# Performance work log

Measured on AMD Instinct MI355X. Metric: run time of the kernel, lower is better.

## Reference

```python
import jax, jax.numpy as jnp
import numpy as np

B, S, D = 2, 2048, 1024
H, DA, DL = 8, 64, 64   # heads, attention_dim, linear_dim
L = 2                    # num_blocks


def _layernorm(x, w, b, eps):
    mu = jnp.mean(x, axis=-1, keepdims=True)
    var = jnp.mean(jnp.square(x - mu), axis=-1, keepdims=True)
    return (x - mu) * jax.lax.rsqrt(var + eps) * w + b


def _norm_no_affine(x, eps):
    mu = jnp.mean(x, axis=-1, keepdims=True)
    var = jnp.mean(jnp.square(x - mu), axis=-1, keepdims=True)
    return (x - mu) * jax.lax.rsqrt(var + eps)


def setup_inputs() -> dict:
    key = jax.random.key(0)
    ks = jax.random.split(key, 8)
    x = jax.random.normal(ks[0], (B, S, D), dtype=jnp.float32)
    # causal visibility mask: True = visible
    attn_mask = jnp.tril(jnp.ones((S, S), dtype=bool))[None].repeat(B, axis=0)
    proj_dim = DL * 2 * H + DA * 2 * H  # 2048
    uvqk = jax.random.normal(ks[1], (L, D, proj_dim), dtype=jnp.float32) * 0.02
    o_w = jax.random.normal(ks[2], (L, D, DL * H), dtype=jnp.float32) * 0.02  # torch [out,in]
    o_b = jnp.zeros((L, D), dtype=jnp.float32)
    ln_w = jnp.ones((L, D), dtype=jnp.float32)
    ln_b = jnp.zeros((L, D), dtype=jnp.float32)
    last_ln_w = jnp.ones((D,), dtype=jnp.float32)
    last_ln_b = jnp.zeros((D,), dtype=jnp.float32)
    return {"x": x, "attn_mask": attn_mask, "uvqk": uvqk, "o_w": o_w,
            "o_b": o_b, "ln_w": ln_w, "ln_b": ln_b,
            "last_ln_w": last_ln_w, "last_ln_b": last_ln_b}


def reference(x, attn_mask, uvqk, o_w, o_b, ln_w, ln_b, last_ln_w, last_ln_b):
    seq_len = x.shape[1]
    m = attn_mask[:, None, :, :]  # [B,1,S,S]
    for i in range(L):
        h = _layernorm(x, ln_w[i], ln_b[i], 1e-6)                 # [B,S,D]
        proj = jax.nn.silu(jnp.einsum('bsd,de->bse', h, uvqk[i]))  # [B,S,2*(DL+DA)*H]
        u, v, q, k = jnp.split(proj, [DL * H, 2 * DL * H, 2 * DL * H + DA * H], axis=-1)
        q = q.reshape(B, seq_len, H, DA).transpose(0, 2, 1, 3)   # [B,H,S,DA]
        kk = k.reshape(B, seq_len, H, DA).transpose(0, 2, 1, 3)
        vv = v.reshape(B, seq_len, H, DL).transpose(0, 2, 1, 3)  # [B,H,S,DL]
        uu = u.reshape(B, seq_len, H, DL).transpose(0, 2, 1, 3)
        scores = jnp.einsum('bhsd,bhtd->bhst', q, kk)            # [B,H,S,S]
        scores = jnp.where(m, jax.nn.silu(scores) / seq_len, 0.0)
        out = jnp.einsum('bhst,bhtd->bhsd', scores, vv)          # [B,H,S,DL]
        out = _norm_no_affine(out, 1e-6)
        u_dot = (uu * out).transpose(0, 2, 1, 3).reshape(B, seq_len, DL * H)
        x = x + jnp.einsum('bsf,df->bsd', u_dot, o_w[i]) + o_b[i]
    return _layernorm(x, last_ln_w, last_ln_b, 1e-8)
```

## Files before the change

### kernel.cpp

```cpp
#include <hip/hip_runtime.h>

#define B_ 2
#define S_ 2048
#define D_ 1024
#define H_ 8
#define L_ 2
#define P_ 2048
#define F_ 512
#define R_ (B_*S_)

typedef unsigned short u16;
typedef unsigned int u32;
typedef __bf16 bf16;
typedef bf16 bf16x8 __attribute__((ext_vector_type(8)));
typedef short short8 __attribute__((ext_vector_type(8)));
typedef float v4f __attribute__((ext_vector_type(4)));

__device__ __forceinline__ float silu_fast(float x){
  float e = __expf(-x);
  return x * __builtin_amdgcn_rcpf(1.0f + e);
}
__device__ __forceinline__ float bf2f(u16 u){
  union { u32 i; float f; } x; x.i = ((u32)u) << 16; return x.f;
}
__device__ __forceinline__ u16 f2bfu(float f){
  union { float f; u32 i; } x; x.f = f;
  u32 r = x.i + 0x7fff + ((x.i >> 16) & 1);
  return (u16)(r >> 16);
}
__device__ __forceinline__ void gload16(const u16* g, u16* l){
  __builtin_amdgcn_global_load_lds(
      (const __attribute__((address_space(1))) void*)g,
      (__attribute__((address_space(3))) void*)l, 16, 0, 0);
}

__global__ __launch_bounds__(256) void cvt_bf16_kernel(const float* __restrict__ src, u16* __restrict__ dst){
  int i = (blockIdx.x * 256 + threadIdx.x) * 4;
  float4 v = *(const float4*)(src + i);
  ushort4 o; o.x = f2bfu(v.x); o.y = f2bfu(v.y); o.z = f2bfu(v.z); o.w = f2bfu(v.w);
  *(ushort4*)(dst + i) = o;
}

__global__ __launch_bounds__(256) void cvt_uvqkT_kernel(const float* __restrict__ uvqk, u16* __restrict__ ot){
  __shared__ float t[32][33];
  int l = blockIdx.z;
  int p0 = blockIdx.x * 32, d0 = blockIdx.y * 32;
  int tx = threadIdx.x & 31, ty = threadIdx.x >> 5;
  const float* src = uvqk + ((size_t)l * D_ + d0) * P_ + p0;
  #pragma unroll
  for (int s = 0; s < 4; s++)
    t[ty + s*8][tx] = src[(size_t)(ty + s*8) * P_ + tx];
  __syncthreads();
  u16* dst = ot + ((size_t)l * P_ + p0) * D_ + d0;
  #pragma unroll
  for (int s = 0; s < 4; s++)
    dst[(size_t)(ty + s*8) * D_ + tx] = f2bfu(t[tx][ty + s*8]);
}

__global__ __launch_bounds__(256) void kvpack_kernel(const u16* __restrict__ projh,
    u16* __restrict__ kpack, u16* __restrict__ vpack){
  __shared__ u16 tls[64*72];
  int t = blockIdx.x, t0 = t * 64;
  int bh = blockIdx.y;
  int b = bh >> 3, hh = bh & 7;
  int tid = threadIdx.x;
  const size_t bS = (size_t)b * S_;
  const int voff = F_ + hh*64, koff = 3*F_ + hh*64;
  {
    int row = tid >> 2, c16 = (tid & 3) * 16;
    const u16* sp = projh + (bS + t0 + row) * P_ + voff + c16;
    short8 a = *(const short8*)sp;
    short8 bq = *(const short8*)(sp + 8);
    *(short8*)&tls[row*72 + c16] = a;
    *(short8*)&tls[row*72 + c16 + 8] = bq;
  }
  __syncthreads();
  size_t obase = ((size_t)(bh*32 + t) * 8) * 512;
  #pragma unroll
  for (int pass = 0; pass < 2; pass++){
    int id = tid + pass * 256;
    int c = id >> 6, lane = id & 63;
    int quad = lane >> 4, l15 = lane & 15;
    int cns = c >> 1, ckst = c & 1;
    const u16* kp = projh + (bS + t0 + cns*16 + l15) * P_ + koff + ckst*32 + quad*8;
    *(short8*)(kpack + obase + (size_t)c*512 + lane*8) = *(const short8*)kp;
    short8 vv;
    #pragma unroll
    for (int j = 0; j < 8; j++)
      vv[j] = (short)tls[(ckst*32 + quad*8 + j)*72 + cns*16 + l15];
    *(short8*)(vpack + obase + (size_t)c*512 + lane*8) = vv;
  }
}

__global__ __launch_bounds__(256) void ln_kernel(const float* __restrict__ src,
    const float* __restrict__ w, const float* __restrict__ b,
    void* __restrict__ outp, float eps, int out_bf16){
  int row = blockIdx.x, tid = threadIdx.x;
  const float* xr = src + (size_t)row * D_;
  float4 v = *(const float4*)(xr + tid * 4);
  float s  = v.x + v.y + v.z + v.w;
  float sq = v.x*v.x + v.y*v.y + v.z*v.z + v.w*v.w;
  #pragma unroll
  for (int off = 32; off; off >>= 1){ s += __shfl_down(s, off); sq += __shfl_down(sq, off); }
  __shared__ float red[8];
  __shared__ float stats[2];
  int wid = tid >> 6;
  if ((tid & 63) == 0){ red[wid] = s; red[4 + wid] = sq; }
  __syncthreads();
  if (tid == 0){
    float S1 = red[0] + red[1] + red[2] + red[3];
    float S2 = red[4] + red[5] + red[6] + red[7];
    float mu = S1 * (1.0f / D_);
    float var = S2 * (1.0f / D_) - mu * mu;
    stats[0] = mu; stats[1] = rsqrtf(var + eps);
  }
  __syncthreads();
  float mu = stats[0], rs = stats[1];
  int i = tid * 4;
  float4 wv = *(const float4*)(w + i);
  float4 bv = *(const float4*)(b + i);
  float o0 = (v.x - mu) * rs * wv.x + bv.x;
  float o1 = (v.y - mu) * rs * wv.y + bv.y;
  float o2 = (v.z - mu) * rs * wv.z + bv.z;
  float o3 = (v.w - mu) * rs * wv.w + bv.w;
  if (out_bf16){
    ushort4 o; o.x = f2bfu(o0); o.y = f2bfu(o1); o.z = f2bfu(o2); o.w = f2bfu(o3);
    *(ushort4*)((u16*)outp + (size_t)row * D_ + i) = o;
  } else {
    *(float4*)((float*)outp + (size_t)row * D_ + i) = make_float4(o0, o1, o2, o3);
  }
}

template<int KDIM>
__device__ __forceinline__ void gemm_mfma_core(const u16* __restrict__ A,
    const u16* __restrict__ Bt, u16* As, u16* Bs, int m0, int n0, v4f acc[4][4]){
  int tid = threadIdx.x;
  int w = tid >> 6, lane = tid & 63;
  int wm = w >> 1, wn = w & 1, quad = lane >> 4, l15 = lane & 15;
  int srow = lane >> 2, skoct = (lane & 3) * 8;
  for (int kt = 0; kt < KDIM; kt += 32){
    __syncthreads();
    #pragma unroll
    for (int s = 0; s < 2; s++){
      int g = w * 2 + s;
      gload16(A  + (size_t)(m0 + g*16 + srow) * KDIM + kt + skoct, As + g*512);
      gload16(Bt + (size_t)(n0 + g*16 + srow) * KDIM + kt + skoct, Bs + g*512);
    }
    __syncthreads();
    short8 af[4], bfr[4];
    #pragma unroll
    for (int i = 0; i < 4; i++)
      af[i] = *(const short8*)&As[(wm*64 + i*16 + l15)*32 + quad*8];
    #pragma unroll
    for (int j = 0; j < 4; j++)
      bfr[j] = *(const short8*)&Bs[(wn*64 + j*16 + l15)*32 + quad*8];
    #pragma unroll
    for (int i = 0; i < 4; i++)
      #pragma unroll
      for (int j = 0; j < 4; j++)
        acc[i][j] = __builtin_amdgcn_mfma_f32_16x16x32_bf16(
            __builtin_bit_cast(bf16x8, af[i]), __builtin_bit_cast(bf16x8, bfr[j]),
            acc[i][j], 0, 0, 0);
  }
}

__global__ __launch_bounds__(256) void gemm_silu_mfma(const u16* __restrict__ A,
    const u16* __restrict__ Bt, u16* __restrict__ C){
  __shared__ u16 As[128*32], Bs[128*32];
  v4f acc[4][4];
  #pragma unroll
  for (int i = 0; i < 4; i++)
    #pragma unroll
    for (int j = 0; j < 4; j++) acc[i][j] = (v4f){0.f,0.f,0.f,0.f};
  int f = blockIdx.x;
  int wg = (f & 7) * 64 + (f >> 3);
  int bx = wg & 15, by = wg >> 4;
  int m0 = by * 128, n0 = bx * 128;
  gemm_mfma_core<D_>(A, Bt, As, Bs, m0, n0, acc);
  int tid = threadIdx.x, w = tid >> 6, lane = tid & 63;
  int wm = w >> 1, wn = w & 1, quad = lane >> 4, l15 = lane & 15;
  #pragma unroll
  for (int i = 0; i < 4; i++)
    #pragma unroll
    for (int r = 0; r < 4; r++){
      int m = m0 + wm*64 + i*16 + quad*4 + r;
      u16* cp = C + (size_t)m * P_ + n0 + wn*64 + l15;
      #pragma unroll
      for (int j = 0; j < 4; j++)
        cp[j*16] = f2bfu(silu_fast(acc[i][j][r]));
    }
}

__global__ __launch_bounds__(256) void gemm_add_mfma(const u16* __restrict__ A,
    const u16* __restrict__ Bt, const float* __restrict__ bias,
    const float* __restrict__ Xin, float* __restrict__ Xout){
  __shared__ u16 As[128*32], Bs[128*32];
  v4f acc[4][4];
  #pragma unroll
  for (int i = 0; i < 4; i++)
    #pragma unroll
    for (int j = 0; j < 4; j++) acc[i][j] = (v4f){0.f,0.f,0.f,0.f};
  int f = blockIdx.x;
  int wg = (f & 7) * 32 + (f >> 3);
  int bx = wg & 7, by = wg >> 3;
  int m0 = by * 128, n0 = bx * 128;
  gemm_mfma_core<F_>(A, Bt, As, Bs, m0, n0, acc);
  int tid = threadIdx.x, w = tid >> 6, lane = tid & 63;
  int wm = w >> 1, wn = w & 1, quad = lane >> 4, l15 = lane & 15;
  float bj[4];
  #pragma unroll
  for (int j = 0; j < 4; j++) bj[j] = bias[n0 + wn*64 + j*16 + l15];
  #pragma unroll
  for (int i = 0; i < 4; i++)
    #pragma unroll
    for (int r = 0; r < 4; r++){
      int m = m0 + wm*64 + i*16 + quad*4 + r;
      size_t off = (size_t)m * D_ + n0 + wn*64 + l15;
      const float* xi = Xin + off;
      float* xo = Xout + off;
      #pragma unroll
      for (int j = 0; j < 4; j++)
        xo[j*16] = xi[j*16] + acc[i][j][r] + bj[j];
    }
}

__global__ __launch_bounds__(256) void attn_kernel(const u16* __restrict__ projh,
                                                   const u16* __restrict__ kpack,
                                                   const u16* __restrict__ vpack,
                                                   u16* __restrict__ opart){
  __shared__ u16 Ps[64*72];
  int f = (int)blockIdx.x;
  int g = f & 7;
  int s = f >> 3;
  int c = s & 31;
  int slot = s >> 5;
  int z = c >> 4;
  int x = c & 15;
  int qt = slot ? x : (15 - x);
  int bh = g + (slot << 3);
  int ttop = 2*qt + 1;
  int b = bh >> 3, hh = bh & 7;
  int tid = threadIdx.x;
  int w = tid >> 6, lane = tid & 63, quad = lane >> 4, l15 = lane & 15;
  int s0 = qt * 128;
  const size_t bS = (size_t)b * S_;
  const int qoff = 2*F_ + hh*64;

  bf16x8 aq[2][2];
  #pragma unroll
  for (int qh = 0; qh < 2; qh++){
    const u16* qp = projh + (bS + s0 + qh*64 + w*16 + l15) * P_ + qoff + quad*8;
    aq[qh][0] = __builtin_bit_cast(bf16x8, *(const short8*)qp);
    aq[qh][1] = __builtin_bit_cast(bf16x8, *(const short8*)(qp + 32));
  }

  v4f oacc[2][4];
  #pragma unroll
  for (int qh = 0; qh < 2; qh++)
    #pragma unroll
    for (int i = 0; i < 4; i++) oacc[qh][i] = (v4f){0.f, 0.f, 0.f, 0.f};

  auto LOADT = [&](short8 (&BK)[4][2], short8 (&VF)[4][2], int tt){
    size_t pb = ((size_t)(bh*32 + tt) * 8) * 512;
    #pragma unroll
    for (int cc = 0; cc < 8; cc++){
      BK[cc>>1][cc&1] = *(const short8*)(kpack + pb + (size_t)cc*512 + lane*8);
      VF[cc>>1][cc&1] = *(const short8*)(vpack + pb + (size_t)cc*512 + lane*8);
    }
  };

  auto COMPUTE = [&](const short8 (&BK)[4][2], const short8 (&VF)[4][2], int t){
    #pragma unroll
    for (int qh = 0; qh < 2; qh++){
      int dtile = 2*qt + qh;
      if (t > dtile) continue;
      v4f sacc[4];
      #pragma unroll
      for (int i = 0; i < 4; i++) sacc[i] = (v4f){0.f, 0.f, 0.f, 0.f};
      #pragma unroll
      for (int ns = 0; ns < 4; ns++){
        sacc[ns] = __builtin_amdgcn_mfma_f32_16x16x32_bf16(aq[qh][0],
            __builtin_bit_cast(bf16x8, BK[ns][0]), sacc[ns], 0, 0, 0);
        sacc[ns] = __builtin_amdgcn_mfma_f32_16x16x32_bf16(aq[qh][1],
            __builtin_bit_cast(bf16x8, BK[ns][1]), sacc[ns], 0, 0, 0);
      }
      bool diag = (t == dtile);
      #pragma unroll
      for (int ns = 0; ns < 4; ns++){
        #pragma unroll
        for (int r = 0; r < 4; r++){
          int rl = w*16 + quad*4 + r;
          int cl = ns*16 + l15;
          float p = silu_fast(sacc[ns][r]) * (1.0f / S_);
          if (diag && cl > rl) p = 0.0f;
          Ps[rl*72 + cl] = f2bfu(p);
        }
      }
      #pragma unroll
      for (int kst = 0; kst < 2; kst++){
        short8 aps = *(const short8*)&Ps[(w*16 + l15)*72 + kst*32 + quad*8];
        bf16x8 ap = __builtin_bit_cast(bf16x8, aps);
        #pragma unroll
        for (int ds = 0; ds < 4; ds++)
          oacc[qh][ds] = __builtin_amdgcn_mfma_f32_16x16x32_bf16(
              ap, __builtin_bit_cast(bf16x8, VF[ds][kst]), oacc[qh][ds], 0, 0, 0);
      }
    }
  };

  short8 kA[4][2], vA[4][2], kB[4][2], vB[4][2];
  int t = z;
  LOADT(kA, vA, t);
  for (;;){
    if (t + 2 <= ttop){
      LOADT(kB, vB, t + 2);
      COMPUTE(kA, vA, t);
      t += 2;
    } else {
      COMPUTE(kA, vA, t);
      break;
    }
    if (t + 2 <= ttop){
      LOADT(kA, vA, t + 2);
      COMPUTE(kB, vB, t);
      t += 2;
    } else {
      COMPUTE(kB, vB, t);
      break;
    }
  }

  u16* ob = opart + (size_t)z * ((size_t)R_ * F_);
  #pragma unroll
  for (int qh = 0; qh < 2; qh++){
    #pragma unroll
    for (int r = 0; r < 4; r++){
      int sg = s0 + qh*64 + w*16 + quad*4 + r;
      u16* op = ob + (bS + sg) * (size_t)F_ + hh*64 + l15;
      #pragma unroll
      for (int ds = 0; ds < 4; ds++)
        op[ds*16] = f2bfu(oacc[qh][ds][r]);
    }
  }
}

__global__ __launch_bounds__(256) void norm_gate_kernel(const u16* __restrict__ opart,
    const u16* __restrict__ projh, u16* __restrict__ udot){
  int w = threadIdx.x >> 6, lane = threadIdx.x & 63;
  int sg = blockIdx.x * 4 + w;
  int hh = lane >> 3, seg = lane & 7;
  size_t off = (size_t)sg * F_ + hh*64 + seg*8;
  short8 a0 = *(const short8*)(opart + off);
  short8 a1 = *(const short8*)(opart + (size_t)R_ * F_ + off);
  float e[8];
  float s = 0.f, sq = 0.f;
  #pragma unroll
  for (int i = 0; i < 8; i++){
    e[i] = bf2f((u16)a0[i]) + bf2f((u16)a1[i]);
    s += e[i]; sq += e[i]*e[i];
  }
  #pragma unroll
  for (int m = 1; m < 8; m <<= 1){
    s  += __shfl_xor(s, m, 64);
    sq += __shfl_xor(sq, m, 64);
  }
  float mu = s * (1.0f/64.0f);
  float var = sq * (1.0f/64.0f) - mu*mu;
  float rs = rsqrtf(var + 1e-6f);
  const u16* up = projh + (size_t)sg * P_ + hh*64 + seg*8;
  short8 uv = *(const short8*)up;
  short8 ov;
  #pragma unroll
  for (int i = 0; i < 8; i++)
    ov[i] = (short)f2bfu((e[i] - mu) * rs * bf2f((u16)uv[i]));
  *(short8*)(udot + off) = ov;
}

extern "C" void kernel_launch(void* const* d_in, const int* in_sizes, int n_in,
                              void* d_out, int out_size, void* d_ws, size_t ws_size,
                              hipStream_t stream){
  (void)in_sizes; (void)n_in; (void)out_size; (void)ws_size;
  const float* x     = (const float*)d_in[0];
  const float* uvqk  = (const float*)d_in[2];
  const float* o_w   = (const float*)d_in[3];
  const float* o_b   = (const float*)d_in[4];
  const float* ln_w  = (const float*)d_in[5];
  const float* ln_b  = (const float*)d_in[6];
  const float* lln_w = (const float*)d_in[7];
  const float* lln_b = (const float*)d_in[8];
  float* out = (float*)d_out;

  char* ws = (char*)d_ws;
  float* xf    = (float*)ws;
  u16*   h     = (u16*)(ws + (16u<<20));
  u16*   kpack = h;
  u16*   vpack = (u16*)(ws + (20u<<20));
  u16*   udot  = (u16*)(ws + (24u<<20));
  u16*   projh = (u16*)(ws + (28u<<20));
  u16*   uvqkT = (u16*)(ws + (44u<<20));
  u16*   owh   = (u16*)(ws + (52u<<20));
  u16*   opart = (u16*)(ws + (54u<<20));

  cvt_uvqkT_kernel<<<dim3(P_/32, D_/32, L_), 256, 0, stream>>>(uvqk, uvqkT);
  cvt_bf16_kernel<<<L_ * D_ * F_ / 1024, 256, 0, stream>>>(o_w, owh);
  for (int l = 0; l < L_; l++){
    const float* xsrc = (l == 0) ? x : xf;
    ln_kernel<<<R_, 256, 0, stream>>>(xsrc, ln_w + l * D_, ln_b + l * D_, h, 1e-6f, 1);
    gemm_silu_mfma<<<512, 256, 0, stream>>>(
        h, uvqkT + (size_t)l * P_ * D_, projh);
    kvpack_kernel<<<dim3(S_/64, B_*H_), 256, 0, stream>>>(projh, kpack, vpack);
    attn_kernel<<<512, 256, 0, stream>>>(projh, kpack, vpack, opart);
    norm_gate_kernel<<<R_/4, 256, 0, stream>>>(opart, projh, udot);
    gemm_add_mfma<<<256, 256, 0, stream>>>(
        udot, owh + (size_t)l * D_ * F_, o_b + l * D_, xsrc, xf);
  }
  ln_kernel<<<R_, 256, 0, stream>>>(xf, lln_w, lln_b, out, 1e-8f, 0);
}
```

Baseline: 280.1 us.

## Load GEMM operands directly into registers with double buffering, remap blocks per XCD

Replaces the LDS-staged GEMM core (global_load_lds plus two barriers per k-step) with per-wave direct global-to-register loads of MFMA fragments, double-buffered across k-steps so loads overlap compute. It also changes the block-to-tile mapping so each of the 8 XCDs gets a contiguous 2D patch of output tiles, aiming for better L2 reuse. This removes LDS traffic and barriers, but each wave now fetches its own A/B fragments, so there is no intra-block sharing and global/L2 traffic goes up, with strided 16-byte loads per lane.

```diff
diff --git a/kernel.cpp b/kernel.cpp
--- a/kernel.cpp
+++ b/kernel.cpp
@@ -27,11 +27,6 @@
   union { float f; u32 i; } x; x.f = f;
   u32 r = x.i + 0x7fff + ((x.i >> 16) & 1);
   return (u16)(r >> 16);
-}
-__device__ __forceinline__ void gload16(const u16* g, u16* l){
-  __builtin_amdgcn_global_load_lds(
-      (const __attribute__((address_space(1))) void*)g,
-      (__attribute__((address_space(3))) void*)l, 16, 0, 0);
 }
 
 __global__ __launch_bounds__(256) void cvt_bf16_kernel(const float* __restrict__ src, u16* __restrict__ dst){
@@ -132,53 +127,52 @@
 }
 
 template<int KDIM>
-__device__ __forceinline__ void gemm_mfma_core(const u16* __restrict__ A,
-    const u16* __restrict__ Bt, u16* As, u16* Bs, int m0, int n0, v4f acc[4][4]){
-  int tid = threadIdx.x;
-  int w = tid >> 6, lane = tid & 63;
-  int wm = w >> 1, wn = w & 1, quad = lane >> 4, l15 = lane & 15;
-  int srow = lane >> 2, skoct = (lane & 3) * 8;
-  for (int kt = 0; kt < KDIM; kt += 32){
-    __syncthreads();
-    #pragma unroll
-    for (int s = 0; s < 2; s++){
-      int g = w * 2 + s;
-      gload16(A  + (size_t)(m0 + g*16 + srow) * KDIM + kt + skoct, As + g*512);
-      gload16(Bt + (size_t)(n0 + g*16 + srow) * KDIM + kt + skoct, Bs + g*512);
-    }
-    __syncthreads();
-    short8 af[4], bfr[4];
-    #pragma unroll
-    for (int i = 0; i < 4; i++)
-      af[i] = *(const short8*)&As[(wm*64 + i*16 + l15)*32 + quad*8];
-    #pragma unroll
-    for (int j = 0; j < 4; j++)
-      bfr[j] = *(const short8*)&Bs[(wn*64 + j*16 + l15)*32 + quad*8];
+__device__ __forceinline__ void gemm_reg_core(const u16* __restrict__ A,
+    const u16* __restrict__ Bt, int m0w, int n0w, v4f acc[4][4]){
+  int lane = threadIdx.x & 63, quad = lane >> 4, l15 = lane & 15;
+  const u16* ap = A  + (size_t)(m0w + l15) * KDIM + quad*8;
+  const u16* bp = Bt + (size_t)(n0w + l15) * KDIM + quad*8;
+  short8 aA[4], bA[4], aB[4], bB[4];
+  auto LOADK = [&](short8 (&af)[4], short8 (&bf)[4], int kt){
+    #pragma unroll
+    for (int i = 0; i < 4; i++){
+      af[i] = *(const short8*)(ap + (size_t)i*16*KDIM + kt);
+      bf[i] = *(const short8*)(bp + (size_t)i*16*KDIM + kt);
+    }
+  };
+  auto COMP = [&](const short8 (&af)[4], const short8 (&bf)[4]){
     #pragma unroll
     for (int i = 0; i < 4; i++)
       #pragma unroll
       for (int j = 0; j < 4; j++)
         acc[i][j] = __builtin_amdgcn_mfma_f32_16x16x32_bf16(
-            __builtin_bit_cast(bf16x8, af[i]), __builtin_bit_cast(bf16x8, bfr[j]),
+            __builtin_bit_cast(bf16x8, af[i]), __builtin_bit_cast(bf16x8, bf[j]),
             acc[i][j], 0, 0, 0);
+  };
+  LOADK(aA, bA, 0);
+  for (int kt = 0; kt < KDIM; kt += 64){
+    if (kt + 32 < KDIM) LOADK(aB, bB, kt + 32);
+    COMP(aA, bA);
+    if (kt + 64 < KDIM) LOADK(aA, bA, kt + 64);
+    COMP(aB, bB);
   }
 }
 
 __global__ __launch_bounds__(256) void gemm_silu_mfma(const u16* __restrict__ A,
     const u16* __restrict__ Bt, u16* __restrict__ C){
-  __shared__ u16 As[128*32], Bs[128*32];
   v4f acc[4][4];
   #pragma unroll
   for (int i = 0; i < 4; i++)
     #pragma unroll
     for (int j = 0; j < 4; j++) acc[i][j] = (v4f){0.f,0.f,0.f,0.f};
   int f = blockIdx.x;
-  int wg = (f & 7) * 64 + (f >> 3);
-  int bx = wg & 15, by = wg >> 4;
+  int k = f & 7, local = f >> 3;
+  int by = (k & 3) * 8 + (local >> 3);
+  int bx = (k >> 2) * 8 + (local & 7);
   int m0 = by * 128, n0 = bx * 128;
-  gemm_mfma_core<D_>(A, Bt, As, Bs, m0, n0, acc);
   int tid = threadIdx.x, w = tid >> 6, lane = tid & 63;
   int wm = w >> 1, wn = w & 1, quad = lane >> 4, l15 = lane & 15;
+  gemm_reg_core<D_>(A, Bt, m0 + wm*64, n0 + wn*64, acc);
   #pragma unroll
   for (int i = 0; i < 4; i++)
     #pragma unroll
@@ -194,19 +188,19 @@
 __global__ __launch_bounds__(256) void gemm_add_mfma(const u16* __restrict__ A,
     const u16* __restrict__ Bt, const float* __restrict__ bias,
     const float* __restrict__ Xin, float* __restrict__ Xout){
-  __shared__ u16 As[128*32], Bs[128*32];
   v4f acc[4][4];
   #pragma unroll
   for (int i = 0; i < 4; i++)
     #pragma unroll
     for (int j = 0; j < 4; j++) acc[i][j] = (v4f){0.f,0.f,0.f,0.f};
   int f = blockIdx.x;
-  int wg = (f & 7) * 32 + (f >> 3);
-  int bx = wg & 7, by = wg >> 3;
+  int k = f & 7, local = f >> 3;
+  int by = (k & 3) * 8 + (local >> 2);
+  int bx = (k >> 2) * 4 + (local & 3);
   int m0 = by * 128, n0 = bx * 128;
-  gemm_mfma_core<F_>(A, Bt, As, Bs, m0, n0, acc);
   int tid = threadIdx.x, w = tid >> 6, lane = tid & 63;
   int wm = w >> 1, wn = w & 1, quad = lane >> 4, l15 = lane & 15;
+  gemm_reg_core<F_>(A, Bt, m0 + wm*64, n0 + wn*64, acc);
   float bj[4];
   #pragma unroll
   for (int j = 0; j < 4; j++) bj[j] = bias[n0 + wn*64 + j*16 + l15];
```

Result: slower. 375.8 us (+34.2%).

## Split attention by query half instead of key parity and fuse norm-gate epilogue

Applied to the files above, without the earlier changes.

Each attention block now owns one 64-row query tile and walks every key tile up to its diagonal, instead of two blocks splitting alternate key tiles over a 128-row tile and writing partial outputs. Because each block holds the full sum, the per-head layernorm and u-gate run in the epilogue and the separate norm_gate kernel and its partial buffer go away. This removes one launch plus the write and reread of two bf16 partial tensors. The cost is that each block now loads K/V tiles for only 64 query rows, and per-block work is less even across the causal triangle.

```diff
diff --git a/kernel.cpp b/kernel.cpp
--- a/kernel.cpp
+++ b/kernel.cpp
@@ -227,38 +227,35 @@
 __global__ __launch_bounds__(256) void attn_kernel(const u16* __restrict__ projh,
                                                    const u16* __restrict__ kpack,
                                                    const u16* __restrict__ vpack,
-                                                   u16* __restrict__ opart){
+                                                   u16* __restrict__ udot){
   __shared__ u16 Ps[64*72];
   int f = (int)blockIdx.x;
   int g = f & 7;
   int s = f >> 3;
   int c = s & 31;
   int slot = s >> 5;
-  int z = c >> 4;
+  int hx = c >> 4;
   int x = c & 15;
   int qt = slot ? x : (15 - x);
   int bh = g + (slot << 3);
-  int ttop = 2*qt + 1;
+  int dtile = 2*qt + hx;
   int b = bh >> 3, hh = bh & 7;
   int tid = threadIdx.x;
   int w = tid >> 6, lane = tid & 63, quad = lane >> 4, l15 = lane & 15;
-  int s0 = qt * 128;
+  int s0 = qt * 128 + hx * 64;
   const size_t bS = (size_t)b * S_;
   const int qoff = 2*F_ + hh*64;
 
-  bf16x8 aq[2][2];
-  #pragma unroll
-  for (int qh = 0; qh < 2; qh++){
-    const u16* qp = projh + (bS + s0 + qh*64 + w*16 + l15) * P_ + qoff + quad*8;
-    aq[qh][0] = __builtin_bit_cast(bf16x8, *(const short8*)qp);
-    aq[qh][1] = __builtin_bit_cast(bf16x8, *(const short8*)(qp + 32));
-  }
-
-  v4f oacc[2][4];
-  #pragma unroll
-  for (int qh = 0; qh < 2; qh++)
-    #pragma unroll
-    for (int i = 0; i < 4; i++) oacc[qh][i] = (v4f){0.f, 0.f, 0.f, 0.f};
+  bf16x8 aq[2];
+  {
+    const u16* qp = projh + (bS + s0 + w*16 + l15) * P_ + qoff + quad*8;
+    aq[0] = __builtin_bit_cast(bf16x8, *(const short8*)qp);
+    aq[1] = __builtin_bit_cast(bf16x8, *(const short8*)(qp + 32));
+  }
+
+  v4f oacc[4];
+  #pragma unroll
+  for (int i = 0; i < 4; i++) oacc[i] = (v4f){0.f, 0.f, 0.f, 0.f};
 
   auto LOADT = [&](short8 (&BK)[4][2], short8 (&VF)[4][2], int tt){
     size_t pb = ((size_t)(bh*32 + tt) * 8) * 512;
@@ -270,110 +267,82 @@
   };
 
   auto COMPUTE = [&](const short8 (&BK)[4][2], const short8 (&VF)[4][2], int t){
-    #pragma unroll
-    for (int qh = 0; qh < 2; qh++){
-      int dtile = 2*qt + qh;
-      if (t > dtile) continue;
-      v4f sacc[4];
-      #pragma unroll
-      for (int i = 0; i < 4; i++) sacc[i] = (v4f){0.f, 0.f, 0.f, 0.f};
-      #pragma unroll
-      for (int ns = 0; ns < 4; ns++){
-        sacc[ns] = __builtin_amdgcn_mfma_f32_16x16x32_bf16(aq[qh][0],
-            __builtin_bit_cast(bf16x8, BK[ns][0]), sacc[ns], 0, 0, 0);
-        sacc[ns] = __builtin_amdgcn_mfma_f32_16x16x32_bf16(aq[qh][1],
-            __builtin_bit_cast(bf16x8, BK[ns][1]), sacc[ns], 0, 0, 0);
+    v4f sacc[4];
+    #pragma unroll
+    for (int i = 0; i < 4; i++) sacc[i] = (v4f){0.f, 0.f, 0.f, 0.f};
+    #pragma unroll
+    for (int ns = 0; ns < 4; ns++){
+      sacc[ns] = __builtin_amdgcn_mfma_f32_16x16x32_bf16(aq[0],
+          __builtin_bit_cast(bf16x8, BK[ns][0]), sacc[ns], 0, 0, 0);
+      sacc[ns] = __builtin_amdgcn_mfma_f32_16x16x32_bf16(aq[1],
+          __builtin_bit_cast(bf16x8, BK[ns][1]), sacc[ns], 0, 0, 0);
+    }
+    bool diag = (t == dtile);
+    #pragma unroll
+    for (int ns = 0; ns < 4; ns++){
+      #pragma unroll
+      for (int r = 0; r < 4; r++){
+        int rl = w*16 + quad*4 + r;
+        int cl = ns*16 + l15;
+        float p = silu_fast(sacc[ns][r]) * (1.0f / S_);
+        if (diag && cl > rl) p = 0.0f;
+        Ps[rl*72 + cl] = f2bfu(p);
       }
-      bool diag = (t == dtile);
-      #pragma unroll
-      for (int ns = 0; ns < 4; ns++){
-        #pragma unroll
-        for (int r = 0; r < 4; r++){
-          int rl = w*16 + quad*4 + r;
-          int cl = ns*16 + l15;
-          float p = silu_fast(sacc[ns][r]) * (1.0f / S_);
-          if (diag && cl > rl) p = 0.0f;
-          Ps[rl*72 + cl] = f2bfu(p);
-        }
-      }
-      #pragma unroll
-      for (int kst = 0; kst < 2; kst++){
-        short8 aps = *(const short8*)&Ps[(w*16 + l15)*72 + kst*32 + quad*8];
-        bf16x8 ap = __builtin_bit_cast(bf16x8, aps);
-        #pragma unroll
-        for (int ds = 0; ds < 4; ds++)
-          oacc[qh][ds] = __builtin_amdgcn_mfma_f32_16x16x32_bf16(
-              ap, __builtin_bit_cast(bf16x8, VF[ds][kst]), oacc[qh][ds], 0, 0, 0);
-      }
+    }
+    #pragma unroll
+    for (int kst = 0; kst < 2; kst++){
+      short8 aps = *(const short8*)&Ps[(w*16 + l15)*72 + kst*32 + quad*8];
+      bf16x8 ap = __builtin_bit_cast(bf16x8, aps);
+      #pragma unroll
+      for (int ds = 0; ds < 4; ds++)
+        oacc[ds] = __builtin_amdgcn_mfma_f32_16x16x32_bf16(
+            ap, __builtin_bit_cast(bf16x8, VF[ds][kst]), oacc[ds], 0, 0, 0);
     }
   };
 
   short8 kA[4][2], vA[4][2], kB[4][2], vB[4][2];
-  int t = z;
-  LOADT(kA, vA, t);
+  int t = 0;
+  LOADT(kA, vA, 0);
   for (;;){
-    if (t + 2 <= ttop){
-      LOADT(kB, vB, t + 2);
+    if (t + 1 <= dtile){
+      LOADT(kB, vB, t + 1);
       COMPUTE(kA, vA, t);
-      t += 2;
+      t++;
     } else {
       COMPUTE(kA, vA, t);
       break;
     }
-    if (t + 2 <= ttop){
-      LOADT(kA, vA, t + 2);
+    if (t + 1 <= dtile){
+      LOADT(kA, vA, t + 1);
       COMPUTE(kB, vB, t);
-      t += 2;
+      t++;
     } else {
       COMPUTE(kB, vB, t);
       break;
     }
   }
 
-  u16* ob = opart + (size_t)z * ((size_t)R_ * F_);
-  #pragma unroll
-  for (int qh = 0; qh < 2; qh++){
-    #pragma unroll
-    for (int r = 0; r < 4; r++){
-      int sg = s0 + qh*64 + w*16 + quad*4 + r;
-      u16* op = ob + (bS + sg) * (size_t)F_ + hh*64 + l15;
-      #pragma unroll
-      for (int ds = 0; ds < 4; ds++)
-        op[ds*16] = f2bfu(oacc[qh][ds][r]);
-    }
-  }
-}
-
-__global__ __launch_bounds__(256) void norm_gate_kernel(const u16* __restrict__ opart,
-    const u16* __restrict__ projh, u16* __restrict__ udot){
-  int w = threadIdx.x >> 6, lane = threadIdx.x & 63;
-  int sg = blockIdx.x * 4 + w;
-  int hh = lane >> 3, seg = lane & 7;
-  size_t off = (size_t)sg * F_ + hh*64 + seg*8;
-  short8 a0 = *(const short8*)(opart + off);
-  short8 a1 = *(const short8*)(opart + (size_t)R_ * F_ + off);
-  float e[8];
-  float s = 0.f, sq = 0.f;
-  #pragma unroll
-  for (int i = 0; i < 8; i++){
-    e[i] = bf2f((u16)a0[i]) + bf2f((u16)a1[i]);
-    s += e[i]; sq += e[i]*e[i];
-  }
-  #pragma unroll
-  for (int m = 1; m < 8; m <<= 1){
-    s  += __shfl_xor(s, m, 64);
-    sq += __shfl_xor(sq, m, 64);
-  }
-  float mu = s * (1.0f/64.0f);
-  float var = sq * (1.0f/64.0f) - mu*mu;
-  float rs = rsqrtf(var + 1e-6f);
-  const u16* up = projh + (size_t)sg * P_ + hh*64 + seg*8;
-  short8 uv = *(const short8*)up;
-  short8 ov;
-  #pragma unroll
-  for (int i = 0; i < 8; i++)
-    ov[i] = (short)f2bfu((e[i] - mu) * rs * bf2f((u16)uv[i]));
-  *(short8*)(udot + off) = ov;
+  #pragma unroll
+  for (int r = 0; r < 4; r++){
+    int sg = s0 + w*16 + quad*4 + r;
+    float e0 = oacc[0][r], e1 = oacc[1][r], e2 = oacc[2][r], e3 = oacc[3][r];
+    float sm = e0 + e1 + e2 + e3;
+    float sq = e0*e0 + e1*e1 + e2*e2 + e3*e3;
+    #pragma unroll
+    for (int m = 1; m < 16; m <<= 1){
+      sm += __shfl_xor(sm, m, 64);
+      sq += __shfl_xor(sq, m, 64);
+    }
+    float mu = sm * (1.0f/64.0f);
+    float var = sq * (1.0f/64.0f) - mu*mu;
+    float rs = rsqrtf(var + 1e-6f);
+    const u16* up = projh + (bS + sg) * P_ + hh*64 + l15;
+    u16* dp = udot + (bS + sg) * (size_t)F_ + hh*64 + l15;
+    float e[4] = {e0, e1, e2, e3};
+    #pragma unroll
+    for (int ds = 0; ds < 4; ds++)
+      dp[ds*16] = f2bfu((e[ds] - mu) * rs * bf2f(up[ds*16]));
+  }
 }
 
 extern "C" void kernel_launch(void* const* d_in, const int* in_sizes, int n_in,
@@ -399,7 +368,6 @@
   u16*   projh = (u16*)(ws + (28u<<20));
   u16*   uvqkT = (u16*)(ws + (44u<<20));
   u16*   owh   = (u16*)(ws + (52u<<20));
-  u16*   opart = (u16*)(ws + (54u<<20));
 
   cvt_uvqkT_kernel<<<dim3(P_/32, D_/32, L_), 256, 0, stream>>>(uvqk, uvqkT);
   cvt_bf16_kernel<<<L_ * D_ * F_ / 1024, 256, 0, stream>>>(o_w, owh);
@@ -409,8 +377,7 @@
     gemm_silu_mfma<<<512, 256, 0, stream>>>(
         h, uvqkT + (size_t)l * P_ * D_, projh);
     kvpack_kernel<<<dim3(S_/64, B_*H_), 256, 0, stream>>>(projh, kpack, vpack);
-    attn_kernel<<<512, 256, 0, stream>>>(projh, kpack, vpack, opart);
-    norm_gate_kernel<<<R_/4, 256, 0, stream>>>(opart, projh, udot);
+    attn_kernel<<<512, 256, 0, stream>>>(projh, kpack, vpack, udot);
     gemm_add_mfma<<<256, 256, 0, stream>>>(
         udot, owh + (size_t)l * D_ * F_, o_b + l * D_, xsrc, xf);
   }
```

Result: no change. 281.5 us (+0.5%).
